# Kernel tuning notes

Measured on AMD Instinct MI355X. Metric: run time of the kernel, lower is better.

The kernel has to match this reference:

```python
import jax, jax.numpy as jnp
import numpy as np

VOCAB = 128000
SEED = 0
PRIOR_TOKENS = 4
DEPTH = 16
TOP_P = 0.9


def setup_inputs() -> dict:
    key = jax.random.key(0)
    k1, k2 = jax.random.split(key)
    input_ids = jax.random.randint(k1, (32, 2048), 0, VOCAB, dtype=jnp.int64 if jax.config.jax_enable_x64 else jnp.int32)
    logits = jax.random.normal(k2, (32, VOCAB), dtype=jnp.float32)
    return {"input_ids": input_ids, "logits": logits}


def _g_values(prior_ids, depth, vocab):
    # Faithful structure: a deterministic Bernoulli(0.5) table of shape [B, depth, vocab]
    # seeded by (seed, prior_ids[b], depth_index). The original uses sha256+numpy RNG;
    # here we use the idiomatic JAX counterpart (fold_in keyed PRNG).
    base = jax.random.key(SEED)
    d_idx = jnp.arange(depth)

    def per_depth(k_b, i):
        return jax.random.bernoulli(jax.random.fold_in(k_b, i), 0.5, (vocab,))

    def per_batch(p):
        k_b = jax.random.fold_in(base, p.astype(jnp.uint32))
        return jax.vmap(lambda i: per_depth(k_b, i))(d_idx)

    return jax.vmap(per_batch)(prior_ids).astype(jnp.float32)  # [B, depth, V]


def _top_p_sample(probs_b, key, top_p):
    V = probs_b.shape[-1]
    sorted_probs, sorted_idx = jax.lax.top_k(probs_b, V)  # descending
    cum = jnp.cumsum(sorted_probs)
    cutoff = jnp.searchsorted(cum, top_p, side='left')
    keep = jnp.arange(V) <= cutoff  # zero out indices > cutoff (matches [cutoff+1:] = 0)
    sp = jnp.where(keep, sorted_probs, 0.0)
    sp = sp / sp.sum()
    sp = jnp.where(jnp.isfinite(sp), sp, 0.0)
    tok = jax.random.categorical(key, jnp.log(sp))  # multinomial(1)
    return sorted_idx[tok]


def reference(input_ids, logits):
    B, V = logits.shape
    prior_ids = input_ids[:, -PRIOR_TOKENS:].sum(axis=-1)  # [B]
    g = _g_values(prior_ids, DEPTH, V)                     # [B, depth, V]

    probs = jax.nn.softmax(logits, axis=-1)
    for i in range(DEPTH):
        g_i = g[:, i, :]                                   # [B, V]
        g_mass = jnp.sum(g_i * probs, axis=-1, keepdims=True)
        probs = probs * (1.0 + g_i - g_mass)

    sample_keys = jax.random.split(jax.random.key(SEED + 1), B)
    next_tokens = jax.vmap(lambda p, k: _top_p_sample(p, k, TOP_P))(probs, sample_keys)

    scores = jnp.full_like(logits, 1e-05)
    scores = scores.at[jnp.arange(B), next_tokens].set(100000.0)
    return scores
```

## Files before the change

kernel.cpp:

```cpp
#include <hip/hip_runtime.h>
#include <stdint.h>


#define NB 32
#define NV 128000
#define NDEPTH 16
#define NTB 500
#define NCB 125
#define NBINS 512
#define CAP 96256
#define NBLKH 94
#define FPSCALE 17592186044416.0
#define TSCALE  68719476736.0
#define MSCALE 1.152921504606846976e18

typedef unsigned long long u64;

__device__ __forceinline__ uint32_t rotl32(uint32_t v, int r) {
  return __builtin_amdgcn_alignbit(v, v, (32 - r) & 31);
}

__device__ __forceinline__ void tf2x32(uint32_t k0, uint32_t k1,
                                       uint32_t x0, uint32_t x1,
                                       uint32_t &o0, uint32_t &o1) {
  uint32_t ks2 = k0 ^ k1 ^ 0x1BD11BDAu;
  x0 += k0; x1 += k1;
  x0 += x1; x1 = rotl32(x1, 13); x1 ^= x0;
  x0 += x1; x1 = rotl32(x1, 15); x1 ^= x0;
  x0 += x1; x1 = rotl32(x1, 26); x1 ^= x0;
  x0 += x1; x1 = rotl32(x1,  6); x1 ^= x0;
  x0 += k1; x1 += ks2 + 1u;
  x0 += x1; x1 = rotl32(x1, 17); x1 ^= x0;
  x0 += x1; x1 = rotl32(x1, 29); x1 ^= x0;
  x0 += x1; x1 = rotl32(x1, 16); x1 ^= x0;
  x0 += x1; x1 = rotl32(x1, 24); x1 ^= x0;
  x0 += ks2; x1 += k0 + 2u;
  x0 += x1; x1 = rotl32(x1, 13); x1 ^= x0;
  x0 += x1; x1 = rotl32(x1, 15); x1 ^= x0;
  x0 += x1; x1 = rotl32(x1, 26); x1 ^= x0;
  x0 += x1; x1 = rotl32(x1,  6); x1 ^= x0;
  x0 += k0; x1 += k1 + 3u;
  x0 += x1; x1 = rotl32(x1, 17); x1 ^= x0;
  x0 += x1; x1 = rotl32(x1, 29); x1 ^= x0;
  x0 += x1; x1 = rotl32(x1, 16); x1 ^= x0;
  x0 += x1; x1 = rotl32(x1, 24); x1 ^= x0;
  x0 += k1; x1 += ks2 + 4u;
  x0 += x1; x1 = rotl32(x1, 13); x1 ^= x0;
  x0 += x1; x1 = rotl32(x1, 15); x1 ^= x0;
  x0 += x1; x1 = rotl32(x1, 26); x1 ^= x0;
  x0 += x1; x1 = rotl32(x1,  6); x1 ^= x0;
  x0 += ks2; x1 += k0 + 5u;
  o0 = x0; o1 = x1;
}

__device__ __forceinline__ uint32_t random_bits32(uint32_t k0, uint32_t k1, uint32_t i) {
  uint32_t y0, y1;
  tf2x32(k0, k1, 0u, i, y0, y1);
  return y0 ^ y1;
}

__global__ void keys_k(const int* __restrict__ ids, int T,
                       uint32_t* __restrict__ kd, uint32_t* __restrict__ sk) {
  int t = threadIdx.x;
  if (t >= NB) return;
  uint32_t prior = 0;
  for (int q = 0; q < 4; ++q) prior += (uint32_t)ids[(size_t)t * T + (T - 4) + q];
  uint32_t b0, b1;
  tf2x32(0u, 0u, 0u, prior, b0, b1);
  for (int d = 0; d < NDEPTH; ++d) {
    uint32_t y0, y1;
    tf2x32(b0, b1, 0u, (uint32_t)d, y0, y1);
    kd[(t * NDEPTH + d) * 2 + 0] = y0;
    kd[(t * NDEPTH + d) * 2 + 1] = y1;
  }
  uint32_t s0, s1;
  tf2x32(0u, 1u, 0u, (uint32_t)t, s0, s1);
  sk[2 * t + 0] = s0;
  sk[2 * t + 1] = s1;
}

__global__ void gmaskmax_k(const uint32_t* __restrict__ kd, const float* __restrict__ logits,
                           uint16_t* __restrict__ mask, float* __restrict__ pmax,
                           uint32_t* __restrict__ ZR) {
  int blk = blockIdx.x, t = threadIdx.x;
  if (blk < 320) ZR[blk * 256 + t] = 0u;
  int b = blk / NTB, c = blk % NTB;
  uint32_t K0[NDEPTH], K1[NDEPTH];
  #pragma unroll
  for (int d = 0; d < NDEPTH; ++d) {
    K0[d] = kd[b * NDEPTH * 2 + 2 * d];
    K1[d] = kd[b * NDEPTH * 2 + 2 * d + 1];
  }
  uint32_t v = (uint32_t)(c * 256 + t);
  size_t i = (size_t)b * NV + v;
  uint32_t m = 0;
  #pragma unroll
  for (int d = NDEPTH - 1; d >= 0; --d) {
    uint32_t bits = random_bits32(K0[d], K1[d], v);
    m = __builtin_amdgcn_alignbit(m, bits, 31);
  }
  mask[i] = (uint16_t)(m ^ 0xFFFFu);
  float x = logits[i];
  for (int o = 32; o > 0; o >>= 1) x = fmaxf(x, __shfl_xor(x, o));
  __shared__ float wmax[4];
  if ((t & 63) == 0) wmax[t >> 6] = x;
  __syncthreads();
  if (t == 0) pmax[b * NTB + c] = fmaxf(fmaxf(wmax[0], wmax[1]), fmaxf(wmax[2], wmax[3]));
}

__global__ void maxr2_k(const float* __restrict__ pmax, float* __restrict__ mx) {
  int t = threadIdx.x;
  int b = t >> 5, k = t & 31;
  float m = -3.4e38f;
  for (int i = k; i < NTB; i += 32) m = fmaxf(m, pmax[b * NTB + i]);
  for (int o = 16; o > 0; o >>= 1) m = fmaxf(m, __shfl_xor(m, o, 32));
  if (k == 0) mx[b] = m;
}

__global__ void lohist_k(const float* __restrict__ logits, const uint16_t* __restrict__ mask,
                         const float* __restrict__ mx, u64* __restrict__ Hlo) {
  int blk = blockIdx.x, t = threadIdx.x;
  int b = blk / NCB, c = blk % NCB;
  __shared__ u64 h[256];
  h[t] = 0ull;
  __syncthreads();
  float mxb = mx[b];
  size_t base = (size_t)b * NV + (size_t)c * 1024;
  #pragma unroll
  for (int e = 0; e < 4; ++e) {
    size_t i = base + e * 256 + t;
    float x = expf(logits[i] - mxb);
    atomicAdd(&h[mask[i] & 255u], (u64)((double)x * FPSCALE));
  }
  __syncthreads();
  if (h[t]) atomicAdd(&Hlo[b * 256 + t], h[t]);
}

__global__ void faclo_k(const u64* __restrict__ Hlo, u64* __restrict__ Zint,
                        float* __restrict__ zf, float* __restrict__ gm,
                        float* __restrict__ wloTab) {
  int b = blockIdx.x, l = threadIdx.x;
  u64 v[4];
  #pragma unroll
  for (int q = 0; q < 4; ++q) v[q] = Hlo[b * 256 + l + 64 * q];
  u64 zp = v[0] + v[1] + v[2] + v[3];
  for (int o = 32; o > 0; o >>= 1) zp += __shfl_xor(zp, o);
  double Zd = (double)zp * (1.0 / FPSCALE);
  if (l == 0) { Zint[b] = zp; zf[b] = (float)Zd; }
  float base[4], w[4];
  #pragma unroll
  for (int q = 0; q < 4; ++q) {
    base[q] = (float)((double)v[q] * (1.0 / FPSCALE) / Zd);
    w[q] = 1.0f;
  }
  #pragma unroll
  for (int d = 0; d < 8; ++d) {
    double part = 0.0;
    #pragma unroll
    for (int q = 0; q < 4; ++q)
      if (((l + 64 * q) >> d) & 1) part += (double)(base[q] * w[q]);
    for (int o = 32; o > 0; o >>= 1) part += __shfl_xor(part, o);
    float g = (float)part;
    if (l == 0) gm[b * NDEPTH + d] = g;
    #pragma unroll
    for (int q = 0; q < 4; ++q) {
      int bit = ((l + 64 * q) >> d) & 1;
      w[q] *= (1.0f + (float)bit) - g;
    }
  }
  #pragma unroll
  for (int q = 0; q < 4; ++q) wloTab[b * 256 + l + 64 * q] = w[q];
}

__global__ void hihist_k(const float* __restrict__ logits, const uint16_t* __restrict__ mask,
                         const float* __restrict__ mx, const float* __restrict__ wloTab,
                         u64* __restrict__ Thist) {
  int blk = blockIdx.x, t = threadIdx.x;
  int b = blk / NCB, c = blk % NCB;
  __shared__ u64 h[256];
  __shared__ float wl[256];
  h[t] = 0ull;
  wl[t] = wloTab[b * 256 + t];
  __syncthreads();
  float mxb = mx[b];
  size_t base = (size_t)b * NV + (size_t)c * 1024;
  #pragma unroll
  for (int e = 0; e < 4; ++e) {
    size_t i = base + e * 256 + t;
    float x = expf(logits[i] - mxb);
    uint32_t mk = mask[i];
    double prod = (double)x * (double)wl[mk & 255u];
    atomicAdd(&h[mk >> 8], (u64)(prod * TSCALE));
  }
  __syncthreads();
  if (h[t]) atomicAdd(&Thist[b * 256 + t], h[t]);
}

__global__ void fachi_k(const u64* __restrict__ Thist, const u64* __restrict__ Zint,
                        float* __restrict__ gm) {
  int b = blockIdx.x, l = threadIdx.x;
  double Zd = (double)Zint[b] * (1.0 / FPSCALE);
  u64 v[4];
  #pragma unroll
  for (int q = 0; q < 4; ++q) v[q] = Thist[b * 256 + l + 64 * q];
  float base[4], w[4];
  #pragma unroll
  for (int q = 0; q < 4; ++q) {
    base[q] = (float)((double)v[q] * (1.0 / TSCALE) / Zd);
    w[q] = 1.0f;
  }
  #pragma unroll
  for (int d = 8; d < NDEPTH; ++d) {
    double part = 0.0;
    #pragma unroll
    for (int q = 0; q < 4; ++q)
      if (((l + 64 * q) >> (d - 8)) & 1) part += (double)(base[q] * w[q]);
    for (int o = 32; o > 0; o >>= 1) part += __shfl_xor(part, o);
    float g = (float)part;
    if (l == 0) gm[b * NDEPTH + d] = g;
    #pragma unroll
    for (int q = 0; q < 4; ++q) {
      int bit = ((l + 64 * q) >> (d - 8)) & 1;
      w[q] *= (1.0f + (float)bit) - g;
    }
  }
}

__global__ void final_k(const float* __restrict__ logits, const uint16_t* __restrict__ mask,
                        const float* __restrict__ mx, const float* __restrict__ zf,
                        const float* __restrict__ gm, uint32_t* __restrict__ keys,
                        u64* __restrict__ binmass, uint32_t* __restrict__ bincnt) {
  int blk = blockIdx.x, t = threadIdx.x;
  int b = blk / NCB, c = blk % NCB;
  __shared__ float gsh[NDEPTH];
  __shared__ float zsh, msh;
  __shared__ u64 bm[NBINS];
  __shared__ uint32_t bc[NBINS];
  if (t < NDEPTH) gsh[t] = gm[b * NDEPTH + t];
  if (t == 16) zsh = zf[b];
  if (t == 17) msh = mx[b];
  for (int i = t; i < NBINS; i += 256) { bm[i] = 0ull; bc[i] = 0u; }
  __syncthreads();
  size_t base = (size_t)b * NV + (size_t)c * 1024;
  #pragma unroll
  for (int e = 0; e < 4; ++e) {
    size_t i = base + e * 256 + t;
    float p = expf(logits[i] - msh) / zsh;
    uint16_t mk = mask[i];
    #pragma unroll
    for (int d = 0; d < NDEPTH; ++d) {
      float g = (float)((mk >> d) & 1);
      p = p * ((1.0f + g) - gsh[d]);
    }
    uint32_t key = ~__float_as_uint(p);
    keys[i] = key;
    uint32_t bin = key >> 23;
    atomicAdd(&bm[bin], (u64)((double)p * MSCALE));
    atomicAdd(&bc[bin], 1u);
  }
  __syncthreads();
  for (int k = t; k < NBINS; k += 256) {
    if (bc[k]) atomicAdd(&bincnt[b * NBINS + k], bc[k]);
    if (bm[k]) atomicAdd(&binmass[b * NBINS + k], bm[k]);
  }
}

__global__ void binsel_k(const u64* __restrict__ binmass, const uint32_t* __restrict__ bincnt,
                         uint32_t* __restrict__ Kthr, uint32_t* __restrict__ Hlen) {
  int b = blockIdx.x, l = threadIdx.x;
  u64 m[8]; uint32_t c[8];
  #pragma unroll
  for (int r = 0; r < 8; ++r) {
    m[r] = binmass[b * NBINS + l * 8 + r];
    c[r] = bincnt[b * NBINS + l * 8 + r];
  }
  #pragma unroll
  for (int r = 1; r < 8; ++r) { m[r] += m[r - 1]; c[r] += c[r - 1]; }
  u64 lm = m[7]; uint32_t lc = c[7];
  u64 im = lm; uint32_t ic = lc;
  for (int o = 1; o < 64; o <<= 1) {
    u64 nm = __shfl_up(im, o);
    uint32_t nc = __shfl_up(ic, o);
    if (l >= o) { im += nm; ic += nc; }
  }
  u64 baseM = im - lm;
  uint32_t baseC = ic - lc;
  __shared__ uint32_t ccL[NBINS];
  #pragma unroll
  for (int r = 0; r < 8; ++r) ccL[l * 8 + r] = baseC + c[r];
  const u64 thr = (u64)((double)0.9f * MSCALE);
  int localFirst = 8; u64 cmAt = 0ull;
  #pragma unroll
  for (int r = 0; r < 8; ++r) {
    if (localFirst == 8 && baseM + m[r] >= thr) { localFirst = r; cmAt = baseM + m[r]; }
  }
  u64 bal = __ballot(localFirst < 8);
  int selB = NBINS - 2; u64 cmSel = 0ull;
  if (bal) {
    int fl = __ffsll((unsigned long long)bal) - 1;
    int sl = __shfl(localFirst, fl);
    cmSel = __shfl(cmAt, fl);
    selB = fl * 8 + sl;
  }
  __syncthreads();
  if (l == 0) {
    int margin = (cmSel >= thr && (cmSel - thr) > (1ull << 22)) ? 0 : 1;
    int Bs = selB + margin;
    if (Bs > NBINS - 1) Bs = NBINS - 1;
    while (Bs > 0 && ccL[Bs] > CAP) --Bs;
    Kthr[b] = (uint32_t)((((u64)(Bs + 1)) << 23) - 1ull);
    Hlen[b] = ccL[Bs];
  }
}

template<int NCH, int NL>
__launch_bounds__(1024)
__global__ void rscan_t(uint32_t* __restrict__ cnt) {
  const int NE = 256 * NCH;
  int b = blockIdx.x, t = threadIdx.x, l = t & 63, wv = t >> 6;
  uint32_t* cc = cnt + (size_t)b * NE;
  uint32_t loc[NL];
  uint32_t s = 0;
  int base = t * NL;
  #pragma unroll
  for (int j = 0; j < NL; ++j) {
    loc[j] = (base + j < NE) ? cc[base + j] : 0u;
    s += loc[j];
  }
  uint32_t incl = s;
  for (int o = 1; o < 64; o <<= 1) {
    uint32_t n = __shfl_up(incl, o);
    if (l >= o) incl += n;
  }
  __shared__ uint32_t wtot[16], wbase[16];
  if (l == 63) wtot[wv] = incl;
  __syncthreads();
  if (t < 16) {
    uint32_t v = wtot[t], i2 = v;
    for (int o = 1; o < 16; o <<= 1) {
      uint32_t n = __shfl_up(i2, o);
      if (t >= o) i2 += n;
    }
    wbase[t] = i2 - v;
  }
  __syncthreads();
  uint32_t run = wbase[wv] + (incl - s);
  #pragma unroll
  for (int j = 0; j < NL; ++j) {
    if (base + j < NE) { uint32_t o = loc[j]; cc[base + j] = run; run += o; }
  }
}

__global__ void rhist1_k(const uint32_t* __restrict__ keys, const uint32_t* __restrict__ Kthr,
                         uint32_t* __restrict__ cnt) {
  int blk = blockIdx.x, t = threadIdx.x;
  int b = blk / NCB, c = blk % NCB;
  uint32_t KT = Kthr[b];
  __shared__ uint32_t lh[256];
  lh[t] = 0;
  __syncthreads();
  size_t base = (size_t)b * NV + (size_t)c * 1024;
  #pragma unroll
  for (int e = 0; e < 4; ++e) {
    uint32_t k = keys[base + 256 * e + t];
    if (k <= KT) atomicAdd(&lh[k & 255u], 1u);
  }
  __syncthreads();
  cnt[((size_t)b * 256 + t) * NCB + c] = lh[t];
}

__launch_bounds__(256)
__global__ void rscatter1_k(const uint32_t* __restrict__ keys, const uint32_t* __restrict__ Kthr,
                            const uint32_t* __restrict__ cnt, uint2* __restrict__ dst0) {
  int blk = blockIdx.x, t = threadIdx.x;
  int b = blk / NCB, c = blk % NCB;
  uint32_t KT = Kthr[b];
  uint2* d = dst0 + (size_t)b * CAP;
  int w = t >> 6, lane = t & 63;
  __shared__ uint32_t runb[256];
  __shared__ uint32_t wvc[4][256];
  runb[t] = cnt[((size_t)b * 256 + t) * NCB + c];
  size_t base = (size_t)b * NV + (size_t)c * 1024;
  uint32_t el[4];
  #pragma unroll
  for (int e = 0; e < 4; ++e) el[e] = keys[base + 256 * e + t];
  u64 lowmask = (1ull << lane) - 1ull;
  #pragma unroll
  for (int e = 0; e < 4; ++e) {
    wvc[0][t] = 0; wvc[1][t] = 0; wvc[2][t] = 0; wvc[3][t] = 0;
    __syncthreads();
    bool active = el[e] <= KT;
    uint32_t dig = active ? (el[e] & 255u) : 0u;
    u64 act = __ballot(active);
    u64 m = ~0ull;
    #pragma unroll
    for (int bit = 0; bit < 8; ++bit) {
      u64 bb = __ballot((dig >> bit) & 1u);
      m &= ((dig >> bit) & 1u) ? bb : ~bb;
    }
    m &= act;
    uint32_t rank = (uint32_t)__popcll(m & lowmask);
    if (active && rank == 0) wvc[w][dig] = (uint32_t)__popcll(m);
    __syncthreads();
    if (active) {
      uint32_t off = runb[dig] + rank;
      for (int w2 = 0; w2 < w; ++w2) off += wvc[w2][dig];
      d[off] = make_uint2(el[e], (uint32_t)(c * 1024 + 256 * e + t));
    }
    __syncthreads();
    runb[t] += wvc[0][t] + wvc[1][t] + wvc[2][t] + wvc[3][t];
    __syncthreads();
  }
}

__global__ void rhist_k(const uint2* __restrict__ src, const uint32_t* __restrict__ Hlen,
                        uint32_t* __restrict__ cnt, int shift) {
  int blk = blockIdx.x, t = threadIdx.x;
  int b = blk / NBLKH, c = blk % NBLKH;
  uint32_t H = Hlen[b];
  if ((uint32_t)(c * 1024) >= H) { cnt[((size_t)b * 256 + t) * NBLKH + c] = 0u; return; }
  const uint2* s = src + (size_t)b * CAP + (size_t)c * 1024;
  __shared__ uint32_t lh[256];
  lh[t] = 0;
  __syncthreads();
  #pragma unroll
  for (int e = 0; e < 4; ++e) {
    uint32_t idx = (uint32_t)(c * 1024 + 256 * e + t);
    if (idx < H) atomicAdd(&lh[(s[t + 256 * e].x >> shift) & 255u], 1u);
  }
  __syncthreads();
  cnt[((size_t)b * 256 + t) * NBLKH + c] = lh[t];
}

__launch_bounds__(256)
__global__ void rscatter_k(const uint2* __restrict__ src, uint2* __restrict__ dst,
                           const uint32_t* __restrict__ Hlen,
                           const uint32_t* __restrict__ cnt, int shift) {
  int blk = blockIdx.x, t = threadIdx.x;
  int b = blk / NBLKH, c = blk % NBLKH;
  uint32_t H = Hlen[b];
  if ((uint32_t)(c * 1024) >= H) return;
  const uint2* s = src + (size_t)b * CAP + (size_t)c * 1024;
  uint2* d = dst + (size_t)b * CAP;
  int w = t >> 6, lane = t & 63;
  __shared__ uint32_t runb[256];
  __shared__ uint32_t wvc[4][256];
  runb[t] = cnt[((size_t)b * 256 + t) * NBLKH + c];
  uint2 el[4];
  #pragma unroll
  for (int e = 0; e < 4; ++e) el[e] = s[t + 256 * e];
  u64 lowmask = (1ull << lane) - 1ull;
  #pragma unroll
  for (int e = 0; e < 4; ++e) {
    wvc[0][t] = 0; wvc[1][t] = 0; wvc[2][t] = 0; wvc[3][t] = 0;
    __syncthreads();
    bool active = (uint32_t)(c * 1024 + 256 * e + t) < H;
    uint32_t dig = active ? ((el[e].x >> shift) & 255u) : 0u;
    u64 act = __ballot(active);
    u64 m = ~0ull;
    #pragma unroll
    for (int bit = 0; bit < 8; ++bit) {
      u64 bb = __ballot((dig >> bit) & 1u);
      m &= ((dig >> bit) & 1u) ? bb : ~bb;
    }
    m &= act;
    uint32_t rank = (uint32_t)__popcll(m & lowmask);
    if (active && rank == 0) wvc[w][dig] = (uint32_t)__popcll(m);
    __syncthreads();
    if (active) {
      uint32_t off = runb[dig] + rank;
      for (int w2 = 0; w2 < w; ++w2) off += wvc[w2][dig];
      d[off] = el[e];
    }
    __syncthreads();
    runb[t] += wvc[0][t] + wvc[1][t] + wvc[2][t] + wvc[3][t];
    __syncthreads();
  }
}

__global__ void chunks_k(const uint2* __restrict__ sp, const uint32_t* __restrict__ Hlen,
                         double* __restrict__ cs) {
  int blk = blockIdx.x, t = threadIdx.x;
  int b = blk / NBLKH, c = blk % NBLKH;
  uint32_t H = Hlen[b];
  if ((uint32_t)(c * 1024) >= H) { if (t == 0) cs[b * NBLKH + c] = 0.0; return; }
  const uint2* p = sp + (size_t)b * CAP + (size_t)c * 1024;
  double s = 0.0;
  for (int k = t; k < 1024; k += 256) {
    uint32_t idx = (uint32_t)(c * 1024 + k);
    if (idx < H) s += (double)__uint_as_float(~p[k].x);
  }
  __shared__ double red[256];
  red[t] = s; __syncthreads();
  for (int st = 128; st > 0; st >>= 1) {
    if (t < st) red[t] += red[t + st];
    __syncthreads();
  }
  if (t == 0) cs[b * NBLKH + c] = red[0];
}

__launch_bounds__(1024)
__global__ void cutargmax_k(const uint2* __restrict__ sp, const double* __restrict__ cs,
                            const uint32_t* __restrict__ Hlen,
                            const uint32_t* __restrict__ sk, u64* __restrict__ best) {
  int b = blockIdx.x, t = threadIdx.x, l = t & 63, wv = t >> 6;
  const double TOPP = (double)0.9f;
  uint32_t H = Hlen[b];
  __shared__ double sh_base;
  __shared__ int sh_ch;
  __shared__ uint32_t sh_cut;
  __shared__ double wsum[16];
  __shared__ u64 wmx[16];
  __shared__ int kSel;
  if (t == 0) { sh_ch = -1; sh_base = 0.0; sh_cut = H - 1; kSel = 1023; }
  __syncthreads();
  if (wv == 0) {
    double v0 = (l < NBLKH) ? cs[b * NBLKH + l] : 0.0;
    double v1 = (l + 64 < NBLKH) ? cs[b * NBLKH + l + 64] : 0.0;
    double i0 = v0;
    for (int o = 1; o < 64; o <<= 1) { double n = __shfl_up(i0, o); if (l >= o) i0 += n; }
    double T0 = __shfl(i0, 63);
    double i1 = v1;
    for (int o = 1; o < 64; o <<= 1) { double n = __shfl_up(i1, o); if (l >= o) i1 += n; }
    i1 += T0;
    bool h0 = (l < NBLKH) && (i0 >= TOPP);
    bool h1 = (l + 64 < NBLKH) && (i1 >= TOPP);
    u64 b0m = __ballot(h0);
    u64 b1m = __ballot(h1);
    int ch = -1; double bse = 0.0;
    if (b0m) {
      int fl = __ffsll((unsigned long long)b0m) - 1;
      ch = fl; bse = __shfl(i0, fl) - __shfl(v0, fl);
    } else if (b1m) {
      int fl = __ffsll((unsigned long long)b1m) - 1;
      ch = 64 + fl; bse = __shfl(i1, fl) - __shfl(v1, fl);
    }
    if (l == 0) { sh_ch = ch; sh_base = bse; }
  }
  __syncthreads();
  int CH = sh_ch;
  if (CH >= 0) {
    double base = sh_base;
    uint32_t idx = (uint32_t)(CH * 1024 + t);
    double pv = (idx < H) ? (double)__uint_as_float(~sp[(size_t)b * CAP + idx].x) : 0.0;
    double iv = pv;
    for (int o = 1; o < 64; o <<= 1) { double n = __shfl_up(iv, o); if (l >= o) iv += n; }
    if (l == 63) wsum[wv] = iv;
    __syncthreads();
    if (t < 16) {
      double v = wsum[t], i2 = v;
      for (int o = 1; o < 16; o <<= 1) { double n = __shfl_up(i2, o); if (t >= o) i2 += n; }
      wsum[t] = i2 - v;
    }
    __syncthreads();
    double full = base + wsum[wv] + iv;
    double prev = full - pv;
    if (full >= TOPP && prev < TOPP) atomicMin(&kSel, (int)t);
    __syncthreads();
    if (t == 0) sh_cut = (uint32_t)(CH * 1024 + (kSel < 1024 ? kSel : 1023));
  }
  __syncthreads();
  uint32_t c = sh_cut;
  uint32_t k0 = sk[2 * b], k1 = sk[2 * b + 1];
  u64 loc = 0ull;
  for (uint32_t j = (uint32_t)t; j <= c; j += 1024) {
    uint32_t bits = random_bits32(k0, k1, j);
    uint32_t m = bits >> 9;
    float u = (m == 0u) ? 1.17549435e-38f : (float)m * 1.1920928955078125e-7f;
    float gum = -logf(-logf(u));
    float scv = logf(__uint_as_float(~sp[(size_t)b * CAP + j].x)) + gum;
    uint32_t su = __float_as_uint(scv);
    uint32_t ord = (su & 0x80000000u) ? ~su : (su | 0x80000000u);
    u64 pk = ((u64)ord << 32) | (u64)(0xFFFFFFFFu - j);
    loc = (pk > loc) ? pk : loc;
  }
  for (int o = 32; o > 0; o >>= 1) {
    u64 oth = __shfl_xor(loc, o);
    loc = (oth > loc) ? oth : loc;
  }
  if (l == 0) wmx[wv] = loc;
  __syncthreads();
  if (t == 0) {
    u64 m = wmx[0];
    for (int k = 1; k < 16; ++k) m = (wmx[k] > m) ? wmx[k] : m;
    best[b] = m;
  }
}

__global__ void fill_k(float* __restrict__ out) {
  size_t i = (size_t)blockIdx.x * 256 + threadIdx.x;
  out[i] = 1e-5f;
}

__global__ void win_k(const u64* __restrict__ best, const uint2* __restrict__ sp,
                      float* __restrict__ out) {
  int b = threadIdx.x;
  if (b >= NB) return;
  u64 pk = best[b];
  uint32_t j = 0xFFFFFFFFu - (uint32_t)(pk & 0xFFFFFFFFull);
  uint32_t tok = sp[(size_t)b * CAP + j].y;
  out[(size_t)b * NV + tok] = 100000.0f;
}

extern "C" void kernel_launch(void* const* d_in, const int* in_sizes, int n_in,
                              void* d_out, int out_size, void* d_ws, size_t ws_size,
                              hipStream_t stream) {
  const int* ids = (const int*)d_in[0];
  const float* logits = (const float*)d_in[1];
  float* out = (float*)d_out;
  int T = in_sizes[0] / NB;

  char* w = (char*)d_ws;
  uint2*    headA = (uint2*)(w + 0);
  uint2*    headB = (uint2*)(w + 24641536);
  uint32_t* keys  = (uint32_t*)(w + 24641536);
  uint32_t* cnt   = (uint32_t*)(w + 49283072);
  uint16_t* mask  = (uint16_t*)(w + 53379072);
  char* S = w + 61571072;
  float*    pmax    = (float*)(S + 0);
  double*   csum    = (double*)(S + 64000);
  float*    mx      = (float*)(S + 88064);
  float*    zf      = (float*)(S + 88192);
  float*    gm      = (float*)(S + 88320);
  uint32_t* Kthr    = (uint32_t*)(S + 90368);
  uint32_t* Hlen    = (uint32_t*)(S + 90496);
  u64*      Zint    = (u64*)(S + 90624);
  float*    wloTab  = (float*)(S + 90880);
  u64*      best    = (u64*)(S + 123648);
  uint32_t* kd      = (uint32_t*)(S + 123904);
  uint32_t* sk      = (uint32_t*)(S + 128000);
  char* ZR = S + 128256;
  u64*      Hlo     = (u64*)(ZR + 0);
  u64*      Thist   = (u64*)(ZR + 65536);
  u64*      binmass = (u64*)(ZR + 131072);
  uint32_t* bincnt  = (uint32_t*)(ZR + 262144);

  const int BVBLK = NB * NTB;
  const int CBLK  = NB * NCB;

  keys_k<<<1, 64, 0, stream>>>(ids, T, kd, sk);
  gmaskmax_k<<<BVBLK, 256, 0, stream>>>(kd, logits, mask, pmax, (uint32_t*)ZR);
  maxr2_k<<<1, 1024, 0, stream>>>(pmax, mx);
  lohist_k<<<CBLK, 256, 0, stream>>>(logits, mask, mx, Hlo);
  faclo_k<<<NB, 64, 0, stream>>>(Hlo, Zint, zf, gm, wloTab);
  hihist_k<<<CBLK, 256, 0, stream>>>(logits, mask, mx, wloTab, Thist);
  fachi_k<<<NB, 64, 0, stream>>>(Thist, Zint, gm);
  final_k<<<CBLK, 256, 0, stream>>>(logits, mask, mx, zf, gm, keys, binmass, bincnt);
  binsel_k<<<NB, 64, 0, stream>>>(binmass, bincnt, Kthr, Hlen);

  rhist1_k<<<CBLK, 256, 0, stream>>>(keys, Kthr, cnt);
  rscan_t<NCB, 32><<<NB, 1024, 0, stream>>>(cnt);
  rscatter1_k<<<CBLK, 256, 0, stream>>>(keys, Kthr, cnt, headA);

  const uint2* srcs[3] = { headA, headB, headA };
  uint2*       dsts[3] = { headB, headA, headB };
  for (int pass = 0; pass < 3; ++pass) {
    int shift = (pass + 1) * 8;
    rhist_k<<<NB * NBLKH, 256, 0, stream>>>(srcs[pass], Hlen, cnt, shift);
    rscan_t<NBLKH, 24><<<NB, 1024, 0, stream>>>(cnt);
    rscatter_k<<<NB * NBLKH, 256, 0, stream>>>(srcs[pass], dsts[pass], Hlen, cnt, shift);
  }

  chunks_k<<<NB * NBLKH, 256, 0, stream>>>(headB, Hlen, csum);
  cutargmax_k<<<NB, 1024, 0, stream>>>(headB, csum, Hlen, sk, best);
  fill_k<<<BVBLK, 256, 0, stream>>>(out);
  win_k<<<1, 32, 0, stream>>>(best, headB, out);
}
```

Measured before the change: 419.7 us.

## Cache exp values, fuse output fill and chunk sums, drop winner kernel

lohist now stores exp(logit-max) into a workspace buffer. hihist and final_k read that buffer instead of recomputing exp from the logits, and final_k overwrites it in place with the sort keys. The output fill moves into final_k, per-chunk sums are computed inside cutargmax_k, and cutargmax_k writes the winning token itself, which removes the chunks, fill and win kernel launches. The cost is an extra 16MB write in lohist plus reading it back, traded against fewer expf calls and launches. It also relies on the initial out fill being ordered before the winner write across kernels.

```diff
diff --git a/kernel.cpp b/kernel.cpp
--- a/kernel.cpp
+++ b/kernel.cpp
@@ -118,7 +118,8 @@
 }
 
 __global__ void lohist_k(const float* __restrict__ logits, const uint16_t* __restrict__ mask,
-                         const float* __restrict__ mx, u64* __restrict__ Hlo) {
+                         const float* __restrict__ mx, float* __restrict__ ef,
+                         u64* __restrict__ Hlo) {
   int blk = blockIdx.x, t = threadIdx.x;
   int b = blk / NCB, c = blk % NCB;
   __shared__ u64 h[256];
@@ -130,6 +131,7 @@
   for (int e = 0; e < 4; ++e) {
     size_t i = base + e * 256 + t;
     float x = expf(logits[i] - mxb);
+    ef[i] = x;
     atomicAdd(&h[mask[i] & 255u], (u64)((double)x * FPSCALE));
   }
   __syncthreads();
@@ -172,9 +174,8 @@
   for (int q = 0; q < 4; ++q) wloTab[b * 256 + l + 64 * q] = w[q];
 }
 
-__global__ void hihist_k(const float* __restrict__ logits, const uint16_t* __restrict__ mask,
-                         const float* __restrict__ mx, const float* __restrict__ wloTab,
-                         u64* __restrict__ Thist) {
+__global__ void hihist_k(const float* __restrict__ ef, const uint16_t* __restrict__ mask,
+                         const float* __restrict__ wloTab, u64* __restrict__ Thist) {
   int blk = blockIdx.x, t = threadIdx.x;
   int b = blk / NCB, c = blk % NCB;
   __shared__ u64 h[256];
@@ -182,14 +183,12 @@
   h[t] = 0ull;
   wl[t] = wloTab[b * 256 + t];
   __syncthreads();
-  float mxb = mx[b];
   size_t base = (size_t)b * NV + (size_t)c * 1024;
   #pragma unroll
   for (int e = 0; e < 4; ++e) {
     size_t i = base + e * 256 + t;
-    float x = expf(logits[i] - mxb);
     uint32_t mk = mask[i];
-    double prod = (double)x * (double)wl[mk & 255u];
+    double prod = (double)ef[i] * (double)wl[mk & 255u];
     atomicAdd(&h[mk >> 8], (u64)(prod * TSCALE));
   }
   __syncthreads();
@@ -226,26 +225,25 @@
   }
 }
 
-__global__ void final_k(const float* __restrict__ logits, const uint16_t* __restrict__ mask,
-                        const float* __restrict__ mx, const float* __restrict__ zf,
-                        const float* __restrict__ gm, uint32_t* __restrict__ keys,
-                        u64* __restrict__ binmass, uint32_t* __restrict__ bincnt) {
+__global__ void final_k(float* __restrict__ efkeys, const uint16_t* __restrict__ mask,
+                        const float* __restrict__ zf, const float* __restrict__ gm,
+                        u64* __restrict__ binmass, uint32_t* __restrict__ bincnt,
+                        float* __restrict__ out) {
   int blk = blockIdx.x, t = threadIdx.x;
   int b = blk / NCB, c = blk % NCB;
   __shared__ float gsh[NDEPTH];
-  __shared__ float zsh, msh;
+  __shared__ float zsh;
   __shared__ u64 bm[NBINS];
   __shared__ uint32_t bc[NBINS];
   if (t < NDEPTH) gsh[t] = gm[b * NDEPTH + t];
   if (t == 16) zsh = zf[b];
-  if (t == 17) msh = mx[b];
   for (int i = t; i < NBINS; i += 256) { bm[i] = 0ull; bc[i] = 0u; }
   __syncthreads();
   size_t base = (size_t)b * NV + (size_t)c * 1024;
   #pragma unroll
   for (int e = 0; e < 4; ++e) {
     size_t i = base + e * 256 + t;
-    float p = expf(logits[i] - msh) / zsh;
+    float p = efkeys[i] / zsh;
     uint16_t mk = mask[i];
     #pragma unroll
     for (int d = 0; d < NDEPTH; ++d) {
@@ -253,7 +251,8 @@
       p = p * ((1.0f + g) - gsh[d]);
     }
     uint32_t key = ~__float_as_uint(p);
-    keys[i] = key;
+    ((uint32_t*)efkeys)[i] = key;
+    out[i] = 1e-5f;
     uint32_t bin = key >> 23;
     atomicAdd(&bm[bin], (u64)((double)p * MSCALE));
     atomicAdd(&bc[bin], 1u);
@@ -478,34 +477,14 @@
   }
 }
 
-__global__ void chunks_k(const uint2* __restrict__ sp, const uint32_t* __restrict__ Hlen,
-                         double* __restrict__ cs) {
-  int blk = blockIdx.x, t = threadIdx.x;
-  int b = blk / NBLKH, c = blk % NBLKH;
-  uint32_t H = Hlen[b];
-  if ((uint32_t)(c * 1024) >= H) { if (t == 0) cs[b * NBLKH + c] = 0.0; return; }
-  const uint2* p = sp + (size_t)b * CAP + (size_t)c * 1024;
-  double s = 0.0;
-  for (int k = t; k < 1024; k += 256) {
-    uint32_t idx = (uint32_t)(c * 1024 + k);
-    if (idx < H) s += (double)__uint_as_float(~p[k].x);
-  }
-  __shared__ double red[256];
-  red[t] = s; __syncthreads();
-  for (int st = 128; st > 0; st >>= 1) {
-    if (t < st) red[t] += red[t + st];
-    __syncthreads();
-  }
-  if (t == 0) cs[b * NBLKH + c] = red[0];
-}
-
 __launch_bounds__(1024)
-__global__ void cutargmax_k(const uint2* __restrict__ sp, const double* __restrict__ cs,
-                            const uint32_t* __restrict__ Hlen,
-                            const uint32_t* __restrict__ sk, u64* __restrict__ best) {
+__global__ void cutargmax_k(const uint2* __restrict__ sp, const uint32_t* __restrict__ Hlen,
+                            const uint32_t* __restrict__ sk, float* __restrict__ out) {
   int b = blockIdx.x, t = threadIdx.x, l = t & 63, wv = t >> 6;
   const double TOPP = (double)0.9f;
   uint32_t H = Hlen[b];
+  const uint2* bsp = sp + (size_t)b * CAP;
+  __shared__ double csL[NBLKH];
   __shared__ double sh_base;
   __shared__ int sh_ch;
   __shared__ uint32_t sh_cut;
@@ -513,10 +492,22 @@
   __shared__ u64 wmx[16];
   __shared__ int kSel;
   if (t == 0) { sh_ch = -1; sh_base = 0.0; sh_cut = H - 1; kSel = 1023; }
+  for (int c = wv; c < NBLKH; c += 16) {
+    double s = 0.0;
+    if ((uint32_t)(c * 1024) < H) {
+      #pragma unroll
+      for (int q = 0; q < 16; ++q) {
+        uint32_t idx = (uint32_t)(c * 1024 + q * 64 + l);
+        if (idx < H) s += (double)__uint_as_float(~bsp[idx].x);
+      }
+      for (int o = 32; o > 0; o >>= 1) s += __shfl_xor(s, o);
+    }
+    if (l == 0) csL[c] = s;
+  }
   __syncthreads();
   if (wv == 0) {
-    double v0 = (l < NBLKH) ? cs[b * NBLKH + l] : 0.0;
-    double v1 = (l + 64 < NBLKH) ? cs[b * NBLKH + l + 64] : 0.0;
+    double v0 = (l < NBLKH) ? csL[l] : 0.0;
+    double v1 = (l + 64 < NBLKH) ? csL[l + 64] : 0.0;
     double i0 = v0;
     for (int o = 1; o < 64; o <<= 1) { double n = __shfl_up(i0, o); if (l >= o) i0 += n; }
     double T0 = __shfl(i0, 63);
@@ -542,7 +533,7 @@
   if (CH >= 0) {
     double base = sh_base;
     uint32_t idx = (uint32_t)(CH * 1024 + t);
-    double pv = (idx < H) ? (double)__uint_as_float(~sp[(size_t)b * CAP + idx].x) : 0.0;
+    double pv = (idx < H) ? (double)__uint_as_float(~bsp[idx].x) : 0.0;
     double iv = pv;
     for (int o = 1; o < 64; o <<= 1) { double n = __shfl_up(iv, o); if (l >= o) iv += n; }
     if (l == 63) wsum[wv] = iv;
@@ -568,7 +559,7 @@
     uint32_t m = bits >> 9;
     float u = (m == 0u) ? 1.17549435e-38f : (float)m * 1.1920928955078125e-7f;
     float gum = -logf(-logf(u));
-    float scv = logf(__uint_as_float(~sp[(size_t)b * CAP + j].x)) + gum;
+    float scv = logf(__uint_as_float(~bsp[j].x)) + gum;
     uint32_t su = __float_as_uint(scv);
     uint32_t ord = (su & 0x80000000u) ? ~su : (su | 0x80000000u);
     u64 pk = ((u64)ord << 32) | (u64)(0xFFFFFFFFu - j);
@@ -583,23 +574,10 @@
   if (t == 0) {
     u64 m = wmx[0];
     for (int k = 1; k < 16; ++k) m = (wmx[k] > m) ? wmx[k] : m;
-    best[b] = m;
-  }
-}
-
-__global__ void fill_k(float* __restrict__ out) {
-  size_t i = (size_t)blockIdx.x * 256 + threadIdx.x;
-  out[i] = 1e-5f;
-}
-
-__global__ void win_k(const u64* __restrict__ best, const uint2* __restrict__ sp,
-                      float* __restrict__ out) {
-  int b = threadIdx.x;
-  if (b >= NB) return;
-  u64 pk = best[b];
-  uint32_t j = 0xFFFFFFFFu - (uint32_t)(pk & 0xFFFFFFFFull);
-  uint32_t tok = sp[(size_t)b * CAP + j].y;
-  out[(size_t)b * NV + tok] = 100000.0f;
+    uint32_t j = 0xFFFFFFFFu - (uint32_t)(m & 0xFFFFFFFFull);
+    uint32_t tok = bsp[j].y;
+    out[(size_t)b * NV + tok] = 100000.0f;
+  }
 }
 
 extern "C" void kernel_launch(void* const* d_in, const int* in_sizes, int n_in,
@@ -613,12 +591,12 @@
   char* w = (char*)d_ws;
   uint2*    headA = (uint2*)(w + 0);
   uint2*    headB = (uint2*)(w + 24641536);
-  uint32_t* keys  = (uint32_t*)(w + 24641536);
+  float*    efkeys = (float*)(w + 24641536);
+  uint32_t* keys   = (uint32_t*)(w + 24641536);
   uint32_t* cnt   = (uint32_t*)(w + 49283072);
   uint16_t* mask  = (uint16_t*)(w + 53379072);
   char* S = w + 61571072;
   float*    pmax    = (float*)(S + 0);
-  double*   csum    = (double*)(S + 64000);
   float*    mx      = (float*)(S + 88064);
   float*    zf      = (float*)(S + 88192);
   float*    gm      = (float*)(S + 88320);
@@ -626,7 +604,6 @@
   uint32_t* Hlen    = (uint32_t*)(S + 90496);
   u64*      Zint    = (u64*)(S + 90624);
   float*    wloTab  = (float*)(S + 90880);
-  u64*      best    = (u64*)(S + 123648);
   uint32_t* kd      = (uint32_t*)(S + 123904);
   uint32_t* sk      = (uint32_t*)(S + 128000);
   char* ZR = S + 128256;
@@ -641,11 +618,11 @@
   keys_k<<<1, 64, 0, stream>>>(ids, T, kd, sk);
   gmaskmax_k<<<BVBLK, 256, 0, stream>>>(kd, logits, mask, pmax, (uint32_t*)ZR);
   maxr2_k<<<1, 1024, 0, stream>>>(pmax, mx);
-  lohist_k<<<CBLK, 256, 0, stream>>>(logits, mask, mx, Hlo);
+  lohist_k<<<CBLK, 256, 0, stream>>>(logits, mask, mx, efkeys, Hlo);
   faclo_k<<<NB, 64, 0, stream>>>(Hlo, Zint, zf, gm, wloTab);
-  hihist_k<<<CBLK, 256, 0, stream>>>(logits, mask, mx, wloTab, Thist);
+  hihist_k<<<CBLK, 256, 0, stream>>>(efkeys, mask, wloTab, Thist);
   fachi_k<<<NB, 64, 0, stream>>>(Thist, Zint, gm);
-  final_k<<<CBLK, 256, 0, stream>>>(logits, mask, mx, zf, gm, keys, binmass, bincnt);
+  final_k<<<CBLK, 256, 0, stream>>>(efkeys, mask, zf, gm, binmass, bincnt, out);
   binsel_k<<<NB, 64, 0, stream>>>(binmass, bincnt, Kthr, Hlen);
 
   rhist1_k<<<CBLK, 256, 0, stream>>>(keys, Kthr, cnt);
@@ -661,8 +638,5 @@
     rscatter_k<<<NB * NBLKH, 256, 0, stream>>>(srcs[pass], dsts[pass], Hlen, cnt, shift);
   }
 
-  chunks_k<<<NB * NBLKH, 256, 0, stream>>>(headB, Hlen, csum);
-  cutargmax_k<<<NB, 1024, 0, stream>>>(headB, csum, Hlen, sk, best);
-  fill_k<<<BVBLK, 256, 0, stream>>>(out);
-  win_k<<<1, 32, 0, stream>>>(best, headB, out);
-}
+  cutargmax_k<<<NB, 1024, 0, stream>>>(headB, Hlen, sk, out);
+}
```

Result: no change. 419.3 us (-0.1%).
